# Performance work log

Hardware: AMD Instinct MI355X
Metric: run time of the kernel (lower is better)

Reference implementation:

```python
import jax, jax.numpy as jnp
import numpy as np

S_, H_, W_ = 7, 56, 56   # input_resolution
WS = 7                   # window_size
SHIFT = 3                # shift_size
GT = 1                   # gt_num (global tokens per window)
HEADS = 12
EPS = 1e-5


def _rel_pos_index(w):
    # replicates the torch buffer construction (incl. its 3*w-1 / 2*w-1 multipliers)
    coords = np.stack(np.meshgrid(np.arange(w), np.arange(w), np.arange(w), indexing='ij'))
    cf = coords.reshape(3, -1)
    rc = (cf[:, :, None] - cf[:, None, :]).transpose(1, 2, 0).astype(np.int64)
    rc += w - 1
    rc[..., 0] *= 3 * w - 1
    rc[..., 1] *= 2 * w - 1
    return rc.sum(-1)  # (w^3, w^3)


def _attn_mask(S, H, W, w, sh):
    # standard 3D shifted-window mask, built once from static shapes
    img = np.zeros((S, H, W))
    cnt = 0
    sls = (slice(0, -w), slice(-w, -sh), slice(-sh, None))
    for a in sls:
        for b in sls:
            for c in sls:
                img[a, b, c] = cnt
                cnt += 1
    m = img.reshape(S // w, w, H // w, w, W // w, w).transpose(0, 2, 4, 1, 3, 5).reshape(-1, w ** 3)
    d = m[:, None, :] - m[:, :, None]
    return np.where(d != 0, -100.0, 0.0).astype(np.float32)  # (nW, w^3, w^3)


def _ln(x, g, b):
    mu = jnp.mean(x, -1, keepdims=True)
    var = jnp.mean((x - mu) ** 2, -1, keepdims=True)
    return (x - mu) * jax.lax.rsqrt(var + EPS) * g + b


def setup_inputs() -> dict:
    key = jax.random.key(0)
    ks = jax.random.split(key, 7)
    C = 384
    hid = 4 * C
    L = S_ * H_ * W_
    nW = (S_ // WS) * (H_ // WS) * (W_ // WS)
    p = lambda k, shape: jax.random.normal(k, shape, jnp.float32) * 0.02
    return dict(
        x=jax.random.normal(ks[0], (1, L, C), jnp.float32),
        gt=jax.random.normal(ks[1], (nW, GT, C), jnp.float32),
        norm1_g=jnp.ones((C,), jnp.float32), norm1_b=jnp.zeros((C,), jnp.float32),
        qkv_w=p(ks[2], (C, 3 * C)), qkv_b=jnp.zeros((3 * C,), jnp.float32),
        bias_table=p(ks[3], ((2 * WS - 1) ** 3, HEADS)),
        proj_w=p(ks[4], (C, C)), proj_b=jnp.zeros((C,), jnp.float32),
        norm2_g=jnp.ones((C,), jnp.float32), norm2_b=jnp.zeros((C,), jnp.float32),
        fc1_w=p(ks[5], (C, hid)), fc1_b=jnp.zeros((hid,), jnp.float32),
        fc2_w=p(ks[6], (hid, C)), fc2_b=jnp.zeros((C,), jnp.float32),
    )


def _forward(x, gt, norm1_g, norm1_b, qkv_w, qkv_b, bias_table, proj_w, proj_b,
             norm2_g, norm2_b, fc1_w, fc1_b, fc2_w, fc2_b):
    B, L, C = x.shape
    h = HEADS
    d = C // h
    scale = d ** -0.5
    N_ = WS ** 3
    N = N_ + GT
    rpi = _rel_pos_index(WS)
    mask = jnp.asarray(_attn_mask(S_, H_, W_, WS, SHIFT))
    nW = mask.shape[0]

    shortcut = x
    xs = _ln(x, norm1_g, norm1_b).reshape(B, S_, H_, W_, C)
    xs = jnp.roll(xs, (-SHIFT, -SHIFT, -SHIFT), axis=(1, 2, 3))  # cyclic shift
    # window partition -> (B*nW, N_, C)
    xw = xs.reshape(B, S_ // WS, WS, H_ // WS, WS, W_ // WS, WS, C)
    xw = xw.transpose(0, 1, 3, 5, 2, 4, 6, 7).reshape(-1, N_, C)

    # --- WindowAttention with global tokens ---
    xc = jnp.concatenate([gt, xw], axis=1)  # (B*nW, N, C)
    qkv = (xc @ qkv_w + qkv_b).reshape(-1, N, 3, h, d).transpose(2, 0, 3, 1, 4)
    q, k, v = qkv[0] * scale, qkv[1], qkv[2]  # (B*nW, h, N, d)
    attn = jnp.einsum('bhnd,bhmd->bhnm', q, k)
    bias = bias_table[rpi.reshape(-1)].reshape(N_, N_, h).transpose(2, 0, 1)  # (h, N_, N_)
    bias = jnp.pad(bias, ((0, 0), (GT, 0), (GT, 0)))      # zeros on gt rows/cols == original submatrix add
    mpad = jnp.pad(mask, ((0, 0), (GT, 0), (GT, 0)))
    attn = attn + bias[None]
    attn = attn.reshape(B, nW, h, N, N) + mpad[None, :, None]
    attn = jax.nn.softmax(attn.reshape(-1, h, N, N), axis=-1)
    out = jnp.einsum('bhnm,bhmd->bhnd', attn, v).transpose(0, 2, 1, 3).reshape(-1, N, C)
    out = out @ proj_w + proj_b
    gt_out = out[:, :GT]
    xw = out[:, GT:]

    # window reverse + reverse shift
    xs = xw.reshape(B, S_ // WS, H_ // WS, W_ // WS, WS, WS, WS, C)
    xs = xs.transpose(0, 1, 4, 2, 5, 3, 6, 7).reshape(B, S_, H_, W_, C)
    xs = jnp.roll(xs, (SHIFT, SHIFT, SHIFT), axis=(1, 2, 3)).reshape(B, L, C)

    x = shortcut + xs  # drop_path = 0
    y = _ln(x, norm2_g, norm2_b)
    y = jax.nn.gelu(y @ fc1_w + fc1_b, approximate=False) @ fc2_w + fc2_b
    return x + y, gt_out


def reference(x, gt, norm1_g, norm1_b, qkv_w, qkv_b, bias_table, proj_w, proj_b,
              norm2_g, norm2_b, fc1_w, fc1_b, fc2_w, fc2_b):
    return _forward(x, gt, norm1_g, norm1_b, qkv_w, qkv_b, bias_table, proj_w, proj_b,
                    norm2_g, norm2_b, fc1_w, fc1_b, fc2_w, fc2_b)
```

## Files before the change

### kernel.cpp

```cpp
#include <hip/hip_runtime.h>
#include <math.h>

typedef __attribute__((ext_vector_type(8))) short short8;
typedef __attribute__((ext_vector_type(4))) float f32x4;

__device__ __forceinline__ float b2f(short s) {
    unsigned u = ((unsigned)(unsigned short)s) << 16;
    return __builtin_bit_cast(float, u);
}
__device__ __forceinline__ short f2b(float f) {
    unsigned u = __builtin_bit_cast(unsigned, f);
    u += 0x7FFFu + ((u >> 16) & 1u);
    return (short)(u >> 16);
}
__device__ __forceinline__ void gload16(const void* g, void* l) {
    __builtin_amdgcn_global_load_lds(
        (const __attribute__((address_space(1))) unsigned int*)g,
        (__attribute__((address_space(3))) unsigned int*)l, 16, 0, 0);
}

__global__ __launch_bounds__(256) void transpose_w(const float* __restrict__ src,
                                                   short* __restrict__ dst,
                                                   int K, int N) {
    __shared__ short tile[32][33];
    const int kt = blockIdx.y * 32, nt = blockIdx.x * 32;
    const int tx = threadIdx.x & 31, ty = threadIdx.x >> 5;
    #pragma unroll
    for (int i = 0; i < 4; i++) {
        int k = kt + ty + 8 * i, n = nt + tx;
        short v = 0;
        if (k < K && n < N) v = f2b(src[(size_t)k * N + n]);
        tile[ty + 8 * i][tx] = v;
    }
    __syncthreads();
    #pragma unroll
    for (int i = 0; i < 4; i++) {
        int n = nt + ty + 8 * i, k = kt + tx;
        if (n < N && k < K) dst[(size_t)n * K + k] = tile[tx][ty + 8 * i];
    }
}

__global__ void bias_pre(const float* __restrict__ btab, float* __restrict__ btf) {
    int idx = blockIdx.x * 256 + threadIdx.x;
    if (idx >= 12 * 22 * 22 * 64) return;
    int lane = idx & 63, rem = idx >> 6;
    int nb = rem % 22; rem /= 22;
    int rt = rem % 22; int head = rem / 22;
    int j = nb * 16 + (lane & 15);
    int ibase = rt * 16 + (lane >> 4) * 4;
    f32x4 out;
    #pragma unroll
    for (int r = 0; r < 4; r++) {
        int i = ibase + r;
        float v;
        if (j >= 344) v = -1e30f;
        else if (i >= 344 || i == 0 || j == 0) v = 0.f;
        else {
            int ti = i - 1, tj = j - 1;
            int ai = ti / 49, bi = (ti % 49) / 7, ci = ti % 7;
            int aj = tj / 49, bj = (tj % 49) / 7, cj = tj % 7;
            int id3 = (ai - aj + 6) * 20 + (bi - bj + 6) * 13 + (ci - cj + 6);
            v = btab[id3 * 12 + head];
        }
        out[r] = v;
    }
    *(f32x4*)&btf[(size_t)idx * 4] = out;
}

__global__ void gid_pre(unsigned char* __restrict__ gid) {
    int idx = blockIdx.x * 256 + threadIdx.x;
    if (idx >= 64 * 352) return;
    int w = idx / 352, n = idx % 352;
    unsigned char g = 0;
    if (n >= 1 && n < 344) {
        int t = n - 1;
        int a = t / 49, bb = (t % 49) / 7, cc = t % 7;
        int hw = w >> 3, ww = w & 7;
        int h = hw * 7 + bb, wd = ww * 7 + cc;
        int gs = (a < 4) ? 1 : 2;
        int gh = (h < 49) ? 0 : ((h < 53) ? 1 : 2);
        int gw = (wd < 49) ? 0 : ((wd < 53) ? 1 : 2);
        g = (unsigned char)(gs * 9 + gh * 3 + gw);
    }
    gid[idx] = g;
}

__global__ __launch_bounds__(256) void ln1_window(
    const float* __restrict__ x, const float* __restrict__ gt,
    const float* __restrict__ g, const float* __restrict__ b,
    short* __restrict__ xc)
{
    int wid = threadIdx.x >> 6, lane = threadIdx.x & 63;
    int r = blockIdx.x * 4 + wid;
    int w = r / 344, n = r - w * 344;
    if (n == 0) {
        #pragma unroll
        for (int i = 0; i < 6; i++) {
            int c = lane + i * 64;
            xc[(size_t)r * 384 + c] = f2b(gt[(size_t)w * 384 + c]);
        }
        return;
    }
    int t = n - 1;
    int a = t / 49, rm = t - a * 49, bb = rm / 7, cc = rm - bb * 7;
    int hw = w >> 3, ww = w & 7;
    int s = (a < 4) ? a + 3 : a - 4;
    int h = hw * 7 + bb + 3; if (h >= 56) h -= 56;
    int wd = ww * 7 + cc + 3; if (wd >= 56) wd -= 56;
    const float* row = x + (size_t)((s * 56 + h) * 56 + wd) * 384;
    float v[6]; float sum = 0.f;
    #pragma unroll
    for (int i = 0; i < 6; i++) { v[i] = row[lane + i * 64]; sum += v[i]; }
    #pragma unroll
    for (int off = 32; off >= 1; off >>= 1) sum += __shfl_xor(sum, off);
    float mu = sum * (1.0f / 384.0f);
    float vs = 0.f;
    #pragma unroll
    for (int i = 0; i < 6; i++) { float d = v[i] - mu; vs += d * d; }
    #pragma unroll
    for (int off = 32; off >= 1; off >>= 1) vs += __shfl_xor(vs, off);
    float rstd = rsqrtf(vs * (1.0f / 384.0f) + 1e-5f);
    #pragma unroll
    for (int i = 0; i < 6; i++) {
        int c = lane + i * 64;
        float o = (v[i] - mu) * rstd * g[c] + b[c];
        xc[(size_t)r * 384 + c] = f2b(o);
    }
}

__global__ __launch_bounds__(256) void ln2_kernel(
    const float* __restrict__ xn, const float* __restrict__ g,
    const float* __restrict__ b, short* __restrict__ out)
{
    int wid = threadIdx.x >> 6, lane = threadIdx.x & 63;
    int r = blockIdx.x * 4 + wid;
    const float* row = xn + (size_t)r * 384;
    float v[6]; float sum = 0.f;
    #pragma unroll
    for (int i = 0; i < 6; i++) { v[i] = row[lane + i * 64]; sum += v[i]; }
    #pragma unroll
    for (int off = 32; off >= 1; off >>= 1) sum += __shfl_xor(sum, off);
    float mu = sum * (1.0f / 384.0f);
    float vs = 0.f;
    #pragma unroll
    for (int i = 0; i < 6; i++) { float d = v[i] - mu; vs += d * d; }
    #pragma unroll
    for (int off = 32; off >= 1; off >>= 1) vs += __shfl_xor(vs, off);
    float rstd = rsqrtf(vs * (1.0f / 384.0f) + 1e-5f);
    #pragma unroll
    for (int i = 0; i < 6; i++) {
        int c = lane + i * 64;
        float o = (v[i] - mu) * rstd * g[c] + b[c];
        out[(size_t)r * 384 + c] = f2b(o);
    }
}

template<int EPI, bool QS>
__global__ __launch_bounds__(256, 4) void gemm128(
    const short* __restrict__ A, const short* __restrict__ BT,
    const float* __restrict__ bias, void* __restrict__ Out,
    const void* __restrict__ P0, void* __restrict__ P1,
    int M, int N, int K)
{
    __shared__ short As[128 * 64];
    __shared__ short Bs[128 * 64];
    const int m0 = blockIdx.y * 128, n0 = blockIdx.x * 128;
    const int tid = threadIdx.x;
    const int wid = tid >> 6, lane = tid & 63;
    const int wm = wid >> 1, wn = wid & 1;
    const int l15 = lane & 15, quad = lane >> 4;

    f32x4 acc[4][4];
    #pragma unroll
    for (int i = 0; i < 4; i++)
        #pragma unroll
        for (int j = 0; j < 4; j++) acc[i][j] = (f32x4){0.f, 0.f, 0.f, 0.f};

    const int trow = tid >> 3;
    const int cs = tid & 7;
    const int gc = cs ^ (trow & 7);
    const short* Ag[4]; const short* Bg[4];
    #pragma unroll
    for (int j = 0; j < 4; j++) {
        int ar = m0 + j * 32 + trow; if (ar >= M) ar = M - 1;
        Ag[j] = A + (size_t)ar * K + gc * 8;
        Bg[j] = BT + (size_t)(n0 + j * 32 + trow) * K + gc * 8;
    }
    short* AsW[4]; short* BsW[4];
    #pragma unroll
    for (int j = 0; j < 4; j++) {
        AsW[j] = &As[(j * 32 + wid * 8) * 64];
        BsW[j] = &Bs[(j * 32 + wid * 8) * 64];
    }
    int arow[4], brow[4];
    #pragma unroll
    for (int mt = 0; mt < 4; mt++) arow[mt] = wm * 64 + mt * 16 + l15;
    #pragma unroll
    for (int nt = 0; nt < 4; nt++) brow[nt] = wn * 64 + nt * 16 + l15;

    for (int ks = 0; ks < K; ks += 64) {
        #pragma unroll
        for (int j = 0; j < 4; j++) gload16(Ag[j] + ks, AsW[j]);
        #pragma unroll
        for (int j = 0; j < 4; j++) gload16(Bg[j] + ks, BsW[j]);
        __syncthreads();
        #pragma unroll
        for (int ko = 0; ko < 2; ko++) {
            short8 af[4], bf[4];
            #pragma unroll
            for (int mt = 0; mt < 4; mt++)
                af[mt] = *(const short8*)&As[arow[mt] * 64
                         + (((ko * 4 + quad) ^ (l15 & 7)) * 8)];
            #pragma unroll
            for (int nt = 0; nt < 4; nt++)
                bf[nt] = *(const short8*)&Bs[brow[nt] * 64
                         + (((ko * 4 + quad) ^ (l15 & 7)) * 8)];
            #pragma unroll
            for (int mt = 0; mt < 4; mt++)
                #pragma unroll
                for (int nt = 0; nt < 4; nt++)
                    acc[mt][nt] = __builtin_amdgcn_mfma_f32_16x16x32_bf16(
                        af[mt], bf[nt], acc[mt][nt], 0, 0, 0);
        }
        __syncthreads();
    }

    #pragma unroll
    for (int mt = 0; mt < 4; mt++) {
        #pragma unroll
        for (int nt = 0; nt < 4; nt++) {
            #pragma unroll
            for (int r = 0; r < 4; r++) {
                int row = m0 + wm * 64 + mt * 16 + quad * 4 + r;
                int col = n0 + wn * 64 + nt * 16 + l15;
                if (row >= M) continue;
                float v = acc[mt][nt][r] + bias[col];
                if (EPI == 0) {
                    if (QS && col < 384) v *= 0.17677669529663687f;
                    ((short*)Out)[(size_t)row * N + col] = f2b(v);
                } else if (EPI == 1) {
                    float u2 = v * v;
                    float w  = v * fmaf(0.07135481633f, u2, 1.5957691216f);
                    float e  = __expf(w);
                    float t  = __builtin_amdgcn_rcpf(1.0f + e);
                    v = v - v * t;
                    ((short*)Out)[(size_t)row * N + col] = f2b(v);
                } else if (EPI == 2) {
                    int w = row / 344, n = row - w * 344;
                    if (n == 0) {
                        ((float*)P1)[(size_t)w * 384 + col] = v;
                    } else {
                        int t = n - 1;
                        int a = t / 49, rm = t - a * 49;
                        int bb = rm / 7, cc = rm - bb * 7;
                        int hw = w >> 3, ww = w & 7;
                        int s = (a < 4) ? a + 3 : a - 4;
                        int h = hw * 7 + bb + 3; if (h >= 56) h -= 56;
                        int wd = ww * 7 + cc + 3; if (wd >= 56) wd -= 56;
                        size_t td = (size_t)((s * 56 + h) * 56 + wd) * 384 + col;
                        ((float*)Out)[td] = v + ((const float*)P0)[td];
                    }
                } else {
                    v += ((const float*)P0)[(size_t)row * N + col];
                    ((float*)Out)[(size_t)row * N + col] = v;
                }
            }
        }
    }
}

__global__ __launch_bounds__(256) void attn_kernel(
    const short* __restrict__ qkv, const float* __restrict__ btf,
    const unsigned char* __restrict__ gid, short* __restrict__ attn_out)
{
    __shared__ short KT[352 * 40];
    __shared__ short VT[32 * 360];
    __shared__ short Pbuf[4 * 16 * 40];
    __shared__ unsigned char Gs[352];
    const int blk = blockIdx.x;
    const int half = blk & 1, wh = blk >> 1;
    const int w = wh / 12, head = wh - w * 12;
    const int tid = threadIdx.x;
    const int wid = tid >> 6, lane = tid & 63;
    const int l15 = lane & 15, quad = lane >> 4;
    const size_t base = (size_t)w * 344 * 1152 + head * 32;

    for (int c = tid; c < 352 * 4; c += 256) {
        int row = c >> 2, off = (c & 3) * 8;
        short8 v8 = (short8){0,0,0,0,0,0,0,0};
        if (row < 344) v8 = *(const short8*)&qkv[base + 384 + (size_t)row * 1152 + off];
        *(short8*)&KT[row * 40 + off] = v8;
    }
    for (int e = tid; e < 344 * 32; e += 256) {
        int key = e >> 5, dd = e & 31;
        VT[dd * 360 + key] = qkv[base + 768 + (size_t)key * 1152 + dd];
    }
    for (int e = tid; e < 16 * 32; e += 256) {
        int key = 344 + (e >> 5), dd = e & 31;
        VT[dd * 360 + key] = 0;
    }
    for (int e = tid; e < 352; e += 256) Gs[e] = gid[w * 352 + e];
    __syncthreads();

    const float* bh = btf + (size_t)head * (22 * 22 * 256);
    short* Pw = &Pbuf[wid * 640];

    for (int rtl = wid; rtl < 11; rtl += 4) {
        int rt = half * 11 + rtl;
        int mbase = rt * 16;
        int qr = mbase + l15; if (qr > 343) qr = 343;
        short8 af = *(const short8*)&qkv[base + (size_t)qr * 1152 + quad * 8];

        int rg[4]; bool ip[4];
        #pragma unroll
        for (int r = 0; r < 4; r++) {
            int i = mbase + quad * 4 + r;
            rg[r] = Gs[i];
            ip[r] = (i > 0);
        }

        f32x4 o0 = {0.f, 0.f, 0.f, 0.f}, o1 = {0.f, 0.f, 0.f, 0.f};
        float l[4] = {0.f, 0.f, 0.f, 0.f};

        #pragma unroll
        for (int kk = 0; kk < 11; kk++) {
            int nb0 = kk * 2, nb1 = kk * 2 + 1;
            f32x4 b0 = *(const f32x4*)&bh[((size_t)(rt * 22 + nb0) * 64 + lane) * 4];
            f32x4 b1 = *(const f32x4*)&bh[((size_t)(rt * 22 + nb1) * 64 + lane) * 4];
            short8 k0 = *(const short8*)&KT[(nb0 * 16 + l15) * 40 + quad * 8];
            short8 k1 = *(const short8*)&KT[(nb1 * 16 + l15) * 40 + quad * 8];
            f32x4 s0 = __builtin_amdgcn_mfma_f32_16x16x32_bf16(af, k0, b0, 0, 0, 0);
            f32x4 s1 = __builtin_amdgcn_mfma_f32_16x16x32_bf16(af, k1, b1, 0, 0, 0);

            int j0 = nb0 * 16 + l15;
            int cg0 = Gs[j0], cg1 = Gs[j0 + 16];
            bool jp0 = (j0 > 0);
            #pragma unroll
            for (int r = 0; r < 4; r++) {
                float s0r = s0[r], s1r = s1[r];
                if (jp0 && ip[r] && rg[r] != cg0) s0r -= 100.0f;
                if (ip[r] && rg[r] != cg1) s1r -= 100.0f;
                float p0 = __expf(s0r);
                float p1 = __expf(s1r);
                l[r] += p0 + p1;
                Pw[(quad * 4 + r) * 40 + l15] = f2b(p0);
                Pw[(quad * 4 + r) * 40 + 16 + l15] = f2b(p1);
            }
            short8 pa = *(const short8*)&Pw[l15 * 40 + quad * 8];
            short8 v0 = *(const short8*)&VT[l15 * 360 + kk * 32 + quad * 8];
            short8 v1 = *(const short8*)&VT[(16 + l15) * 360 + kk * 32 + quad * 8];
            o0 = __builtin_amdgcn_mfma_f32_16x16x32_bf16(pa, v0, o0, 0, 0, 0);
            o1 = __builtin_amdgcn_mfma_f32_16x16x32_bf16(pa, v1, o1, 0, 0, 0);
        }

        #pragma unroll
        for (int r = 0; r < 4; r++) {
            l[r] += __shfl_xor(l[r], 1);
            l[r] += __shfl_xor(l[r], 2);
            l[r] += __shfl_xor(l[r], 4);
            l[r] += __shfl_xor(l[r], 8);
        }
        #pragma unroll
        for (int r = 0; r < 4; r++) {
            int row = mbase + quad * 4 + r;
            if (row < 344) {
                float inv = 1.0f / l[r];
                size_t ob = ((size_t)w * 344 + row) * 384 + head * 32;
                attn_out[ob + l15] = f2b(o0[r] * inv);
                attn_out[ob + 16 + l15] = f2b(o1[r] * inv);
            }
        }
    }
}

extern "C" void kernel_launch(void* const* d_in, const int* in_sizes, int n_in,
                              void* d_out, int out_size, void* d_ws, size_t ws_size,
                              hipStream_t stream)
{
    const float* x      = (const float*)d_in[0];
    const float* gt     = (const float*)d_in[1];
    const float* n1g    = (const float*)d_in[2];
    const float* n1b    = (const float*)d_in[3];
    const float* qkv_w  = (const float*)d_in[4];
    const float* qkv_b  = (const float*)d_in[5];
    const float* btab   = (const float*)d_in[6];
    const float* proj_w = (const float*)d_in[7];
    const float* proj_b = (const float*)d_in[8];
    const float* n2g    = (const float*)d_in[9];
    const float* n2b    = (const float*)d_in[10];
    const float* fc1_w  = (const float*)d_in[11];
    const float* fc1_b  = (const float*)d_in[12];
    const float* fc2_w  = (const float*)d_in[13];
    const float* fc2_b  = (const float*)d_in[14];

    char* ws = (char*)d_ws;
    short* wt_qkv  = (short*)(ws + 0);
    short* wt_proj = (short*)(ws + 884736);
    short* wt_fc1  = (short*)(ws + 1179648);
    short* wt_fc2  = (short*)(ws + 2359296);
    short* xc      = (short*)(ws + 3538944);
    short* qkvb    = (short*)(ws + 20447232);
    short* attn_o  = xc;
    short* h1      = (short*)(ws + 3538944);
    float* xnew    = (float*)(ws + 71172096);
    float* btf     = (float*)(ws + 71172096);
    unsigned char* gidb = (unsigned char*)(ws + 77119488);
    short* xnorm   = (short*)(ws + 104890368);

    float* outx  = (float*)d_out;
    float* outgt = outx + (size_t)21952 * 384;

    transpose_w<<<dim3(36, 12), 256, 0, stream>>>(qkv_w, wt_qkv, 384, 1152);
    transpose_w<<<dim3(12, 12), 256, 0, stream>>>(proj_w, wt_proj, 384, 384);
    transpose_w<<<dim3(48, 12), 256, 0, stream>>>(fc1_w, wt_fc1, 384, 1536);
    transpose_w<<<dim3(12, 48), 256, 0, stream>>>(fc2_w, wt_fc2, 1536, 384);

    bias_pre<<<dim3((12 * 22 * 22 * 64 + 255) / 256), 256, 0, stream>>>(btab, btf);
    gid_pre<<<dim3((64 * 352 + 255) / 256), 256, 0, stream>>>(gidb);

    ln1_window<<<dim3(5504), 256, 0, stream>>>(x, gt, n1g, n1b, xc);

    gemm128<0, true><<<dim3(9, 172), 256, 0, stream>>>(xc, wt_qkv, qkv_b, qkvb,
                                                       nullptr, nullptr, 22016, 1152, 384);

    attn_kernel<<<dim3(1536), 256, 0, stream>>>(qkvb, btf, gidb, attn_o);

    gemm128<2, false><<<dim3(3, 172), 256, 0, stream>>>(attn_o, wt_proj, proj_b, xnew,
                                                        x, outgt, 22016, 384, 384);

    ln2_kernel<<<dim3(5488), 256, 0, stream>>>(xnew, n2g, n2b, xnorm);

    gemm128<1, false><<<dim3(12, 172), 256, 0, stream>>>(xnorm, wt_fc1, fc1_b, h1,
                                                         nullptr, nullptr, 21952, 1536, 384);

    gemm128<3, false><<<dim3(3, 172), 256, 0, stream>>>(h1, wt_fc2, fc2_b, outx,
                                                        xnew, nullptr, 21952, 384, 1536);
}
```

Before: 428.6 us.

## Process two query tiles per wave in attention, swizzle LDS, halve block count

The attention kernel now runs one block per window-head instead of two halves. Each wave handles two 16-row query tiles at once, so every K and V fragment read from LDS feeds two MFMAs. This removes the duplicate K/V staging that the two half-blocks did before. K and P buffers move from padded to XOR-swizzled layouts, and V is loaded as 16-byte vectors. The mask now zeroes probabilities after exp instead of subtracting 100 before, and P is rounded with a cheaper bf16 conversion. In exchange, register pressure rises, fewer blocks may leave CUs underfilled (11 tiles across 4 waves is uneven), and the masking semantics change slightly.

Result: no change. 428.1 us (-0.1%).

```diff
diff --git a/kernel.cpp b/kernel.cpp
--- a/kernel.cpp
+++ b/kernel.cpp
@@ -12,6 +12,10 @@
     unsigned u = __builtin_bit_cast(unsigned, f);
     u += 0x7FFFu + ((u >> 16) & 1u);
     return (short)(u >> 16);
+}
+__device__ __forceinline__ short f2bf(float f) {
+    unsigned u = __builtin_bit_cast(unsigned, f);
+    return (short)((u + 0x8000u) >> 16);
 }
 __device__ __forceinline__ void gload16(const void* g, void* l) {
     __builtin_amdgcn_global_load_lds(
@@ -273,29 +277,31 @@
     const short* __restrict__ qkv, const float* __restrict__ btf,
     const unsigned char* __restrict__ gid, short* __restrict__ attn_out)
 {
-    __shared__ short KT[352 * 40];
+    __shared__ short KT[352 * 32];
     __shared__ short VT[32 * 360];
-    __shared__ short Pbuf[4 * 16 * 40];
+    __shared__ short Pbuf[4 * 2 * 16 * 32];
     __shared__ unsigned char Gs[352];
     const int blk = blockIdx.x;
-    const int half = blk & 1, wh = blk >> 1;
-    const int w = wh / 12, head = wh - w * 12;
+    const int w = blk / 12, head = blk - w * 12;
     const int tid = threadIdx.x;
     const int wid = tid >> 6, lane = tid & 63;
     const int l15 = lane & 15, quad = lane >> 4;
     const size_t base = (size_t)w * 344 * 1152 + head * 32;
 
     for (int c = tid; c < 352 * 4; c += 256) {
-        int row = c >> 2, off = (c & 3) * 8;
+        int row = c >> 2, ch = c & 3;
         short8 v8 = (short8){0,0,0,0,0,0,0,0};
-        if (row < 344) v8 = *(const short8*)&qkv[base + 384 + (size_t)row * 1152 + off];
-        *(short8*)&KT[row * 40 + off] = v8;
-    }
-    for (int e = tid; e < 344 * 32; e += 256) {
-        int key = e >> 5, dd = e & 31;
-        VT[dd * 360 + key] = qkv[base + 768 + (size_t)key * 1152 + dd];
-    }
-    for (int e = tid; e < 16 * 32; e += 256) {
+        if (row < 344) v8 = *(const short8*)&qkv[base + 384 + (size_t)row * 1152 + ch * 8];
+        int slot = ch ^ ((row >> 1) & 3);
+        *(short8*)&KT[row * 32 + slot * 8] = v8;
+    }
+    for (int e = tid; e < 344 * 4; e += 256) {
+        int key = e >> 2, g = (e & 3) * 8;
+        short8 v8 = *(const short8*)&qkv[base + 768 + (size_t)key * 1152 + g];
+        #pragma unroll
+        for (int i = 0; i < 8; i++) VT[(g + i) * 360 + key] = v8[i];
+    }
+    for (int e = tid; e < 8 * 32; e += 256) {
         int key = 344 + (e >> 5), dd = e & 31;
         VT[dd * 360 + key] = 0;
     }
@@ -303,71 +309,99 @@
     __syncthreads();
 
     const float* bh = btf + (size_t)head * (22 * 22 * 256);
-    short* Pw = &Pbuf[wid * 640];
-
-    for (int rtl = wid; rtl < 11; rtl += 4) {
-        int rt = half * 11 + rtl;
-        int mbase = rt * 16;
-        int qr = mbase + l15; if (qr > 343) qr = 343;
-        short8 af = *(const short8*)&qkv[base + (size_t)qr * 1152 + quad * 8];
-
-        int rg[4]; bool ip[4];
+    short* PwA = &Pbuf[wid * 1024];
+    short* PwB = PwA + 512;
+
+    const int cl = l15 & 7, c0 = l15 >> 3, c1 = c0 | 2;
+    const int sw0 = (quad * 2) & 3, sw1 = sw0 | 1;
+    const int swq = (l15 >> 1) & 3;
+    const int paOff = l15 * 32 + ((quad ^ swq) * 8);
+    const int ktOff = l15 * 32 + ((quad ^ swq) * 8);
+    const int o0r01 = ((c0 ^ sw0) * 8) + cl, o0r23 = ((c0 ^ sw1) * 8) + cl;
+    const int o1r01 = ((c1 ^ sw0) * 8) + cl, o1r23 = ((c1 ^ sw1) * 8) + cl;
+
+    for (int j = wid; j < 11; j += 4) {
+        const int rtA = 2 * j, rtB = rtA + 1;
+        const int qrA = rtA * 16 + l15;
+        int qrB = rtB * 16 + l15; if (qrB > 343) qrB = 343;
+        short8 afA = *(const short8*)&qkv[base + (size_t)qrA * 1152 + quad * 8];
+        short8 afB = *(const short8*)&qkv[base + (size_t)qrB * 1152 + quad * 8];
+
+        int rgA[4], rgB[4]; bool ipA[4];
         #pragma unroll
         for (int r = 0; r < 4; r++) {
-            int i = mbase + quad * 4 + r;
-            rg[r] = Gs[i];
-            ip[r] = (i > 0);
-        }
-
-        f32x4 o0 = {0.f, 0.f, 0.f, 0.f}, o1 = {0.f, 0.f, 0.f, 0.f};
-        float l[4] = {0.f, 0.f, 0.f, 0.f};
-
-        #pragma unroll
+            int iA = rtA * 16 + quad * 4 + r;
+            rgA[r] = Gs[iA]; ipA[r] = (iA > 0);
+            rgB[r] = Gs[iA + 16];
+        }
+
+        f32x4 oA0 = {0,0,0,0}, oA1 = {0,0,0,0}, oB0 = {0,0,0,0}, oB1 = {0,0,0,0};
+        float lA[4] = {0,0,0,0}, lB[4] = {0,0,0,0};
+        const float* bhA = bh + (size_t)rtA * (22 * 256);
+        const float* bhB = bh + (size_t)rtB * (22 * 256);
+
         for (int kk = 0; kk < 11; kk++) {
-            int nb0 = kk * 2, nb1 = kk * 2 + 1;
-            f32x4 b0 = *(const f32x4*)&bh[((size_t)(rt * 22 + nb0) * 64 + lane) * 4];
-            f32x4 b1 = *(const f32x4*)&bh[((size_t)(rt * 22 + nb1) * 64 + lane) * 4];
-            short8 k0 = *(const short8*)&KT[(nb0 * 16 + l15) * 40 + quad * 8];
-            short8 k1 = *(const short8*)&KT[(nb1 * 16 + l15) * 40 + quad * 8];
-            f32x4 s0 = __builtin_amdgcn_mfma_f32_16x16x32_bf16(af, k0, b0, 0, 0, 0);
-            f32x4 s1 = __builtin_amdgcn_mfma_f32_16x16x32_bf16(af, k1, b1, 0, 0, 0);
-
-            int j0 = nb0 * 16 + l15;
+            const int nb0 = kk * 2, nb1 = nb0 + 1;
+            f32x4 bA0 = *(const f32x4*)&bhA[(size_t)(nb0 * 64 + lane) * 4];
+            f32x4 bA1 = *(const f32x4*)&bhA[(size_t)(nb1 * 64 + lane) * 4];
+            f32x4 bB0 = *(const f32x4*)&bhB[(size_t)(nb0 * 64 + lane) * 4];
+            f32x4 bB1 = *(const f32x4*)&bhB[(size_t)(nb1 * 64 + lane) * 4];
+            short8 k0 = *(const short8*)&KT[nb0 * 512 + ktOff];
+            short8 k1 = *(const short8*)&KT[nb1 * 512 + ktOff];
+            f32x4 sA0 = __builtin_amdgcn_mfma_f32_16x16x32_bf16(afA, k0, bA0, 0, 0, 0);
+            f32x4 sA1 = __builtin_amdgcn_mfma_f32_16x16x32_bf16(afA, k1, bA1, 0, 0, 0);
+            f32x4 sB0 = __builtin_amdgcn_mfma_f32_16x16x32_bf16(afB, k0, bB0, 0, 0, 0);
+            f32x4 sB1 = __builtin_amdgcn_mfma_f32_16x16x32_bf16(afB, k1, bB1, 0, 0, 0);
+
+            int j0 = kk * 32 + l15;
             int cg0 = Gs[j0], cg1 = Gs[j0 + 16];
             bool jp0 = (j0 > 0);
             #pragma unroll
             for (int r = 0; r < 4; r++) {
-                float s0r = s0[r], s1r = s1[r];
-                if (jp0 && ip[r] && rg[r] != cg0) s0r -= 100.0f;
-                if (ip[r] && rg[r] != cg1) s1r -= 100.0f;
-                float p0 = __expf(s0r);
-                float p1 = __expf(s1r);
-                l[r] += p0 + p1;
-                Pw[(quad * 4 + r) * 40 + l15] = f2b(p0);
-                Pw[(quad * 4 + r) * 40 + 16 + l15] = f2b(p1);
+                float pA0 = __expf(sA0[r]); if (jp0 && ipA[r] && rgA[r] != cg0) pA0 = 0.f;
+                float pA1 = __expf(sA1[r]); if (ipA[r] && rgA[r] != cg1) pA1 = 0.f;
+                float pB0 = __expf(sB0[r]); if (jp0 && rgB[r] != cg0) pB0 = 0.f;
+                float pB1 = __expf(sB1[r]); if (rgB[r] != cg1) pB1 = 0.f;
+                lA[r] += pA0 + pA1;
+                lB[r] += pB0 + pB1;
+                int rowb = (quad * 4 + r) * 32;
+                int oo0 = (r < 2) ? o0r01 : o0r23;
+                int oo1 = (r < 2) ? o1r01 : o1r23;
+                PwA[rowb + oo0] = f2bf(pA0);
+                PwA[rowb + oo1] = f2bf(pA1);
+                PwB[rowb + oo0] = f2bf(pB0);
+                PwB[rowb + oo1] = f2bf(pB1);
             }
-            short8 pa = *(const short8*)&Pw[l15 * 40 + quad * 8];
+            short8 paA = *(const short8*)&PwA[paOff];
+            short8 paB = *(const short8*)&PwB[paOff];
             short8 v0 = *(const short8*)&VT[l15 * 360 + kk * 32 + quad * 8];
             short8 v1 = *(const short8*)&VT[(16 + l15) * 360 + kk * 32 + quad * 8];
-            o0 = __builtin_amdgcn_mfma_f32_16x16x32_bf16(pa, v0, o0, 0, 0, 0);
-            o1 = __builtin_amdgcn_mfma_f32_16x16x32_bf16(pa, v1, o1, 0, 0, 0);
+            oA0 = __builtin_amdgcn_mfma_f32_16x16x32_bf16(paA, v0, oA0, 0, 0, 0);
+            oA1 = __builtin_amdgcn_mfma_f32_16x16x32_bf16(paA, v1, oA1, 0, 0, 0);
+            oB0 = __builtin_amdgcn_mfma_f32_16x16x32_bf16(paB, v0, oB0, 0, 0, 0);
+            oB1 = __builtin_amdgcn_mfma_f32_16x16x32_bf16(paB, v1, oB1, 0, 0, 0);
         }
 
         #pragma unroll
         for (int r = 0; r < 4; r++) {
-            l[r] += __shfl_xor(l[r], 1);
-            l[r] += __shfl_xor(l[r], 2);
-            l[r] += __shfl_xor(l[r], 4);
-            l[r] += __shfl_xor(l[r], 8);
+            lA[r] += __shfl_xor(lA[r], 1); lA[r] += __shfl_xor(lA[r], 2);
+            lA[r] += __shfl_xor(lA[r], 4); lA[r] += __shfl_xor(lA[r], 8);
+            lB[r] += __shfl_xor(lB[r], 1); lB[r] += __shfl_xor(lB[r], 2);
+            lB[r] += __shfl_xor(lB[r], 4); lB[r] += __shfl_xor(lB[r], 8);
         }
         #pragma unroll
         for (int r = 0; r < 4; r++) {
-            int row = mbase + quad * 4 + r;
-            if (row < 344) {
-                float inv = 1.0f / l[r];
-                size_t ob = ((size_t)w * 344 + row) * 384 + head * 32;
-                attn_out[ob + l15] = f2b(o0[r] * inv);
-                attn_out[ob + 16 + l15] = f2b(o1[r] * inv);
+            int rowA = rtA * 16 + quad * 4 + r;
+            float invA = 1.0f / lA[r];
+            size_t obA = ((size_t)w * 344 + rowA) * 384 + head * 32;
+            attn_out[obA + l15] = f2b(oA0[r] * invA);
+            attn_out[obA + 16 + l15] = f2b(oA1[r] * invA);
+            int rowB = rowA + 16;
+            if (rowB < 344) {
+                float invB = 1.0f / lB[r];
+                size_t obB = ((size_t)w * 344 + rowB) * 384 + head * 32;
+                attn_out[obB + l15] = f2b(oB0[r] * invB);
+                attn_out[obB + 16 + l15] = f2b(oB1[r] * invB);
             }
         }
     }
@@ -423,7 +457,7 @@
     gemm128<0, true><<<dim3(9, 172), 256, 0, stream>>>(xc, wt_qkv, qkv_b, qkvb,
                                                        nullptr, nullptr, 22016, 1152, 384);
 
-    attn_kernel<<<dim3(1536), 256, 0, stream>>>(qkvb, btf, gidb, attn_o);
+    attn_kernel<<<dim3(768), 256, 0, stream>>>(qkvb, btf, gidb, attn_o);
 
     gemm128<2, false><<<dim3(3, 172), 256, 0, stream>>>(attn_o, wt_proj, proj_b, xnew,
                                                         x, outgt, 22016, 384, 384);
```
